# Kernel optimization log

Measured on AMD Instinct MI355X. Metric: run time of the kernel, lower is better.

The kernel has to match this reference:

```python
import jax, jax.numpy as jnp
import numpy as np

N_NODES = 50000
N_EDGES = 800000
D = 128
N_GRAPHS = 64


def setup_inputs() -> dict:
    key = jax.random.key(0)
    ks = jax.random.split(key, 9)
    x = jax.random.normal(ks[0], (N_NODES, D), dtype=jnp.float32)
    edge_index = jax.random.randint(ks[1], (2, N_EDGES), 0, N_NODES, dtype=jnp.int32)
    batch = jnp.sort(jax.random.randint(ks[2], (N_NODES,), 0, N_GRAPHS, dtype=jnp.int32))
    s = 1.0 / np.sqrt(D)
    W1 = jax.random.normal(ks[3], (D, D), jnp.float32) * s
    W2 = jax.random.normal(ks[4], (D, D), jnp.float32) * s
    W3 = jax.random.normal(ks[5], (D, D), jnp.float32) * s
    b1 = jnp.zeros((D,), jnp.float32)
    b2 = jnp.zeros((D,), jnp.float32)
    b3 = jnp.zeros((D,), jnp.float32)
    return {"x": x, "W1": W1, "b1": b1, "W2": W2, "b2": b2, "W3": W3, "b3": b3,
            "edge_index": edge_index, "batch": batch}


def _gcn_conv(x, W, b, src, dst, deg_inv_sqrt):
    # PyG GCNConv: x' = D^{-1/2} (A+I) D^{-1/2} (x W) + b
    h = x @ W                                    # [N, D]
    norm = (deg_inv_sqrt[src] * deg_inv_sqrt[dst])[:, None]   # [E, 1]
    agg = jax.ops.segment_sum(h[src] * norm, dst, num_segments=N_NODES)
    # self-loop contribution: norm_ii = deg_i^{-1}
    agg = agg + (deg_inv_sqrt * deg_inv_sqrt)[:, None] * h
    return agg + b


def reference(x, W1, b1, W2, b2, W3, b3, edge_index, batch):
    src, dst = edge_index[0], edge_index[1]
    # degree on A + I (self-loops added), edge weight 1
    deg = jax.ops.segment_sum(jnp.ones((N_EDGES,), x.dtype), dst,
                              num_segments=N_NODES) + 1.0
    deg_inv_sqrt = jax.lax.rsqrt(deg)
    h = jax.nn.relu(_gcn_conv(x, W1, b1, src, dst, deg_inv_sqrt))
    h = jax.nn.relu(_gcn_conv(h, W2, b2, src, dst, deg_inv_sqrt))
    h = _gcn_conv(h, W3, b3, src, dst, deg_inv_sqrt)
    # global_max_pool over graph ids
    return jax.ops.segment_max(h, batch, num_segments=N_GRAPHS)
```

## Files before the change

kernel.cpp:

```cpp
#include <hip/hip_runtime.h>
#include <float.h>
#include <math.h>

#define D 128
#define PCHUNK 64
#define NBUCK 256
#define BROWS 196
#define BCAP 4096
#define BCAPP 4896
#define ACHUNK 3125

typedef _Float16 half8 __attribute__((ext_vector_type(8)));
typedef _Float16 half2v __attribute__((ext_vector_type(2)));
typedef float f32x4 __attribute__((ext_vector_type(4)));

__device__ __forceinline__ unsigned encf(float x) {
    unsigned u = __float_as_uint(x);
    return (u & 0x80000000u) ? ~u : (u | 0x80000000u);
}
__device__ __forceinline__ float decf(unsigned e) {
    unsigned u = (e & 0x80000000u) ? (e & 0x7FFFFFFFu) : ~e;
    return __uint_as_float(u);
}

__global__ __launch_bounds__(256) void binA_kernel(const int* __restrict__ src,
                                                   const int* __restrict__ dst,
                                                   int* __restrict__ gcnt,
                                                   uint2* __restrict__ gpair, int ne) {
    __shared__ int lh[NBUCK], ssc[NBUCK], lstart[NBUCK], gbase[NBUCK], loff[NBUCK];
    __shared__ uint2 stage[ACHUNK + 8];
    int t = threadIdx.x;
    int e0 = blockIdx.x * ACHUNK;
    int e1 = min(e0 + ACHUNK, ne);
    lh[t] = 0;
    __syncthreads();
    for (int e = e0 + t; e < e1; e += 256) atomicAdd(&lh[dst[e] / BROWS], 1);
    __syncthreads();
    ssc[t] = lh[t];
    __syncthreads();
    for (int off = 1; off < NBUCK; off <<= 1) {
        int u = (t >= off) ? ssc[t - off] : 0;
        __syncthreads();
        ssc[t] += u;
        __syncthreads();
    }
    int st = ssc[t] - lh[t];
    lstart[t] = st;
    loff[t] = st;
    if (lh[t] > 0) gbase[t] = atomicAdd(&gcnt[t], lh[t]);
    __syncthreads();
    for (int e = e0 + t; e < e1; e += 256) {
        int s = src[e], d = dst[e];
        int pos = atomicAdd(&loff[d / BROWS], 1);
        stage[pos] = make_uint2((unsigned)s, (unsigned)d);
    }
    __syncthreads();
    int m = e1 - e0;
    for (int i = t; i < m; i += 256) {
        uint2 pr = stage[i];
        int b = (int)pr.y / BROWS;
        int gpos = b * BCAP + gbase[b] + (i - lstart[b]);
        if (gpos < (b + 1) * BCAP) gpair[gpos] = pr;
    }
}

__global__ __launch_bounds__(256) void binB_kernel(const uint2* __restrict__ gpair,
                                                   const int* __restrict__ gcnt,
                                                   int2* __restrict__ rowptr2,
                                                   float* __restrict__ disv,
                                                   int* __restrict__ csr, int n) {
    __shared__ int lh[256], ssc[256], loff[256];
    __shared__ int cstage[BCAPP];
    int b = blockIdx.x, t = threadIdx.x;
    int m = min(gcnt[b], BCAP);
    int row0 = b * BROWS;
    int nrows = min(BROWS, n - row0);
    if (nrows <= 0) return;
    const uint2* mp = gpair + (size_t)b * BCAP;
    lh[t] = 0;
    __syncthreads();
    for (int i = t; i < m; i += 256) atomicAdd(&lh[(int)mp[i].y - row0], 1);
    __syncthreads();
    int deg = lh[t];
    int pdeg = (deg + 3) & ~3;
    ssc[t] = pdeg;
    __syncthreads();
    for (int off = 1; off < 256; off <<= 1) {
        int u = (t >= off) ? ssc[t - off] : 0;
        __syncthreads();
        ssc[t] += u;
        __syncthreads();
    }
    int st = ssc[t] - pdeg;
    loff[t] = st;
    __syncthreads();
    int bbase = b * BCAPP;
    if (t < nrows) {
        rowptr2[row0 + t] = make_int2(bbase + st, deg);
        disv[row0 + t] = rsqrtf((float)deg + 1.0f);
    }
    for (int i = t; i < m; i += 256) {
        uint2 pr = mp[i];
        int pos = atomicAdd(&loff[(int)pr.y - row0], 1);
        cstage[pos] = (int)pr.x;
    }
    if (t < nrows) {
        for (int k = deg; k < pdeg; k++) cstage[st + k] = row0 + t;
    }
    __syncthreads();
    int ptot = ssc[255];
    for (int i = t; i < ptot; i += 256) csr[bbase + i] = cstage[i];
}

__global__ void pack3_kernel(const float* __restrict__ W1, const float* __restrict__ W2,
                             const float* __restrict__ W3, _Float16* __restrict__ Wp1,
                             _Float16* __restrict__ Wp2, _Float16* __restrict__ Wp3,
                             unsigned* __restrict__ outEnc, int nout) {
    int gi = blockIdx.x * blockDim.x + threadIdx.x;
    if (gi < nout) outEnc[gi] = 0x007FFFFFu;
    int w = gi >> 14, i = gi & 16383;
    const float* W = (w == 0) ? W1 : (w == 1) ? W2 : W3;
    _Float16* Wp = (w == 0) ? Wp1 : (w == 1) ? Wp2 : Wp3;
    int j = i & 7, l = (i >> 3) & 63, t = (i >> 9) & 7, s = (i >> 12) & 3;
    int k = s * 32 + ((l >> 4) << 3) + j;
    int c = t * 16 + (l & 15);
    Wp[i] = (_Float16)W[k * 128 + c];
}

template <bool F32SRC>
__global__ __launch_bounds__(256) void gemm_mfma(const void* __restrict__ Xsrc,
                                                 const _Float16* __restrict__ Wp,
                                                 const float* __restrict__ disv,
                                                 _Float16* __restrict__ Gh,
                                                 int ntiles, int n) {
    __shared__ _Float16 Wl[16384];
    int tid = threadIdx.x;
    {
        const uint4* s4 = (const uint4*)Wp;
        uint4* d4 = (uint4*)Wl;
#pragma unroll
        for (int i = 0; i < 8; i++) d4[tid + 256 * i] = s4[tid + 256 * i];
    }
    __syncthreads();
    int wave = tid >> 6, lane = tid & 63;
    int m = lane & 15, quad = lane >> 4;
    const half8* wfrag = (const half8*)Wl;
    const _Float16* Xh = (const _Float16*)Xsrc;
    const float* Xf = (const float*)Xsrc;

#pragma unroll
    for (int pass = 0; pass < 2; pass++) {
        int tile = blockIdx.x * 8 + pass * 4 + wave;
        if (tile >= ntiles) continue;
        int arow = tile * 16 + m;
        if (arow >= n) arow = n - 1;

        f32x4 acc[8];
#pragma unroll
        for (int t = 0; t < 8; t++) acc[t] = (f32x4){0.f, 0.f, 0.f, 0.f};

#pragma unroll
        for (int s = 0; s < 4; s++) {
            half8 a;
            if (F32SRC) {
                float4 lo = *(const float4*)(Xf + (size_t)arow * D + s * 32 + quad * 8);
                float4 hi = *(const float4*)(Xf + (size_t)arow * D + s * 32 + quad * 8 + 4);
                a[0] = (_Float16)lo.x; a[1] = (_Float16)lo.y; a[2] = (_Float16)lo.z; a[3] = (_Float16)lo.w;
                a[4] = (_Float16)hi.x; a[5] = (_Float16)hi.y; a[6] = (_Float16)hi.z; a[7] = (_Float16)hi.w;
            } else {
                a = *(const half8*)(Xh + (size_t)arow * D + s * 32 + quad * 8);
            }
#pragma unroll
            for (int t = 0; t < 8; t++) {
                half8 bf = wfrag[(s * 8 + t) * 64 + lane];
                acc[t] = __builtin_amdgcn_mfma_f32_16x16x32_f16(a, bf, acc[t], 0, 0, 0);
            }
        }
        int orow0 = tile * 16 + quad * 4;
        if (orow0 + 3 < n) {
            float d0 = disv[orow0], d1 = disv[orow0 + 1], d2 = disv[orow0 + 2], d3 = disv[orow0 + 3];
#pragma unroll
            for (int t = 0; t < 8; t++) {
                int col = t * 16 + m;
                Gh[(size_t)(orow0 + 0) * D + col] = (_Float16)(acc[t][0] * d0);
                Gh[(size_t)(orow0 + 1) * D + col] = (_Float16)(acc[t][1] * d1);
                Gh[(size_t)(orow0 + 2) * D + col] = (_Float16)(acc[t][2] * d2);
                Gh[(size_t)(orow0 + 3) * D + col] = (_Float16)(acc[t][3] * d3);
            }
        } else {
#pragma unroll
            for (int t = 0; t < 8; t++) {
                int col = t * 16 + m;
#pragma unroll
                for (int r = 0; r < 4; r++) {
                    int orow = orow0 + r;
                    if (orow < n) Gh[(size_t)orow * D + col] = (_Float16)(acc[t][r] * disv[orow]);
                }
            }
        }
    }
}

__global__ __launch_bounds__(256) void agg_f16(const _Float16* __restrict__ G,
                                               const int2* __restrict__ rowptr2,
                                               const int* __restrict__ csr,
                                               const float* __restrict__ disv,
                                               const float* __restrict__ bias,
                                               _Float16* __restrict__ Out, int n, int relu) {
    int wave = threadIdx.x >> 6, lane = threadIdx.x & 63;
    int node = blockIdx.x * 4 + wave;
    if (node >= n) return;
    int sub = lane >> 4, li = lane & 15;
    const half8* G8 = (const half8*)G;
    int2 rp = rowptr2[node];
    int e0 = rp.x, deg = rp.y;
    int pend = e0 + ((deg + 3) & ~3);
    int npad = pend - e0 - deg;
    float acc[8];
    if (sub == 0) {
        half8 sv = G8[(size_t)node * 16 + li];
        float w = (float)(1 - npad);
#pragma unroll
        for (int j = 0; j < 8; j++) acc[j] = w * (float)sv[j];
    } else {
#pragma unroll
        for (int j = 0; j < 8; j++) acc[j] = 0.f;
    }
    int e = e0;
    for (; e + 16 <= pend; e += 16) {
        int4 ix = *(const int4*)(csr + e + sub * 4);
        half8 v0 = G8[(size_t)ix.x * 16 + li];
        half8 v1 = G8[(size_t)ix.y * 16 + li];
        half8 v2 = G8[(size_t)ix.z * 16 + li];
        half8 v3 = G8[(size_t)ix.w * 16 + li];
#pragma unroll
        for (int j = 0; j < 8; j++)
            acc[j] += ((float)v0[j] + (float)v1[j]) + ((float)v2[j] + (float)v3[j]);
    }
    if (e + 8 <= pend) {
        int2 ix = *(const int2*)(csr + e + sub * 2);
        half8 v0 = G8[(size_t)ix.x * 16 + li];
        half8 v1 = G8[(size_t)ix.y * 16 + li];
#pragma unroll
        for (int j = 0; j < 8; j++) acc[j] += (float)v0[j] + (float)v1[j];
        e += 8;
    }
    if (e < pend) {
        int i0 = csr[e + sub];
        half8 v0 = G8[(size_t)i0 * 16 + li];
#pragma unroll
        for (int j = 0; j < 8; j++) acc[j] += (float)v0[j];
    }
#pragma unroll
    for (int j = 0; j < 8; j++) {
        acc[j] += __shfl_xor(acc[j], 16);
        acc[j] += __shfl_xor(acc[j], 32);
    }
    if (sub == 0) {
        float dd = disv[node];
        float4 b0 = *(const float4*)&bias[li * 8];
        float4 b1 = *(const float4*)&bias[li * 8 + 4];
        float o0 = fmaf(dd, acc[0], b0.x), o1 = fmaf(dd, acc[1], b0.y);
        float o2 = fmaf(dd, acc[2], b0.z), o3 = fmaf(dd, acc[3], b0.w);
        float o4 = fmaf(dd, acc[4], b1.x), o5 = fmaf(dd, acc[5], b1.y);
        float o6 = fmaf(dd, acc[6], b1.z), o7 = fmaf(dd, acc[7], b1.w);
        if (relu) {
            o0 = fmaxf(o0, 0.f); o1 = fmaxf(o1, 0.f); o2 = fmaxf(o2, 0.f); o3 = fmaxf(o3, 0.f);
            o4 = fmaxf(o4, 0.f); o5 = fmaxf(o5, 0.f); o6 = fmaxf(o6, 0.f); o7 = fmaxf(o7, 0.f);
        }
        half8 h;
        h[0] = (_Float16)o0; h[1] = (_Float16)o1; h[2] = (_Float16)o2; h[3] = (_Float16)o3;
        h[4] = (_Float16)o4; h[5] = (_Float16)o5; h[6] = (_Float16)o6; h[7] = (_Float16)o7;
        ((half8*)Out)[(size_t)node * 16 + li] = h;
    }
}

__global__ __launch_bounds__(128) void pool_kernel(const _Float16* __restrict__ H,
                                                   const int* __restrict__ batch,
                                                   unsigned* __restrict__ outEnc, int n) {
    int half = threadIdx.x >> 6;
    int li = threadIdx.x & 63;
    int start = blockIdx.x * PCHUNK + half * (PCHUNK / 2);
    if (start >= n) return;
    int end = min(start + PCHUNK / 2, n);
    int c = li * 2;
    int curg = batch[start];
    float cx = -INFINITY, cy = -INFINITY;
    for (int i = start; i < end; i++) {
        half2v v = *(const half2v*)(H + (size_t)i * D + c);
        float vx = (float)v[0], vy = (float)v[1];
        int g = batch[i];
        if (g != curg) {
            atomicMax(&outEnc[curg * D + c], encf(cx));
            atomicMax(&outEnc[curg * D + c + 1], encf(cy));
            cx = vx; cy = vy; curg = g;
        } else {
            cx = fmaxf(cx, vx); cy = fmaxf(cy, vy);
        }
    }
    atomicMax(&outEnc[curg * D + c], encf(cx));
    atomicMax(&outEnc[curg * D + c + 1], encf(cy));
}

__global__ void decode_kernel(const unsigned* __restrict__ outEnc, float* __restrict__ out, int n) {
    int i = blockIdx.x * blockDim.x + threadIdx.x;
    if (i < n) out[i] = decf(outEnc[i]);
}

extern "C" void kernel_launch(void* const* d_in, const int* in_sizes, int n_in,
                              void* d_out, int out_size, void* d_ws, size_t ws_size,
                              hipStream_t stream) {
    const float* x  = (const float*)d_in[0];
    const float* W1 = (const float*)d_in[1];
    const float* b1 = (const float*)d_in[2];
    const float* W2 = (const float*)d_in[3];
    const float* b2 = (const float*)d_in[4];
    const float* W3 = (const float*)d_in[5];
    const float* b3 = (const float*)d_in[6];
    const int* ei    = (const int*)d_in[7];
    const int* batch = (const int*)d_in[8];

    int n  = in_sizes[0] / D;
    int ne = in_sizes[7] / 2;
    const int* src = ei;
    const int* dst = ei + ne;

    char* p = (char*)d_ws;
    auto alloc = [&](size_t bytes) -> void* {
        void* q = (void*)p;
        p += (bytes + 255) & ~(size_t)255;
        return q;
    };
    _Float16* Gh  = (_Float16*)alloc((size_t)n * D * 2);
    _Float16* Hh  = (_Float16*)alloc((size_t)n * D * 2);
    _Float16* Wp1 = (_Float16*)alloc((size_t)D * D * 2);
    _Float16* Wp2 = (_Float16*)alloc((size_t)D * D * 2);
    _Float16* Wp3 = (_Float16*)alloc((size_t)D * D * 2);
    int* gcnt     = (int*)alloc((size_t)NBUCK * 4);
    uint2* gpair  = (uint2*)alloc((size_t)NBUCK * BCAP * 8);
    int2* rowptr2 = (int2*)alloc((size_t)n * 8);
    int* csr      = (int*)alloc((size_t)NBUCK * BCAPP * 4);
    float* disv   = (float*)alloc((size_t)n * 4);
    unsigned* outEnc = (unsigned*)alloc((size_t)out_size * 4);

    hipMemsetAsync(gcnt, 0, (size_t)NBUCK * 4, stream);

    int nblocksA = (ne + ACHUNK - 1) / ACHUNK;
    binA_kernel<<<nblocksA, 256, 0, stream>>>(src, dst, gcnt, gpair, ne);
    binB_kernel<<<NBUCK, 256, 0, stream>>>(gpair, gcnt, rowptr2, disv, csr, n);
    pack3_kernel<<<192, 256, 0, stream>>>(W1, W2, W3, Wp1, Wp2, Wp3, outEnc, out_size);

    int ntiles = (n + 15) / 16;
    int gemm_blocks = (ntiles + 7) / 8;
    int agg_blocks  = (n + 3) / 4;

    gemm_mfma<true><<<gemm_blocks, 256, 0, stream>>>(x, Wp1, disv, Gh, ntiles, n);
    agg_f16<<<agg_blocks, 256, 0, stream>>>(Gh, rowptr2, csr, disv, b1, Hh, n, 1);
    gemm_mfma<false><<<gemm_blocks, 256, 0, stream>>>(Hh, Wp2, disv, Gh, ntiles, n);
    agg_f16<<<agg_blocks, 256, 0, stream>>>(Gh, rowptr2, csr, disv, b2, Hh, n, 1);
    gemm_mfma<false><<<gemm_blocks, 256, 0, stream>>>(Hh, Wp3, disv, Gh, ntiles, n);
    agg_f16<<<agg_blocks, 256, 0, stream>>>(Gh, rowptr2, csr, disv, b3, Hh, n, 0);

    pool_kernel<<<(n + PCHUNK - 1) / PCHUNK, 128, 0, stream>>>(Hh, batch, outEnc, n);
    decode_kernel<<<(out_size + 255) / 256, 256, 0, stream>>>(outEnc, (float*)d_out, out_size);
}
```

Before: 248.9 us.

## Merge weight packing into binning launch and add nontemporal hints in aggregation

The weight-packing and output-init work moves into extra blocks of the edge-binning kernel, which removes one kernel launch. The aggregation kernel now uses nontemporal loads for CSR indices and row pointers and nontemporal stores for its output and the CSR writes. It also folds the per-node normalisation into the accumulation as FMAs, in place of a final scale. That adds per-element multiplies and changes rounding slightly, and the nontemporal stores on Out may hurt later GEMM reads that could have hit in cache.

```diff
diff --git a/kernel.cpp b/kernel.cpp
--- a/kernel.cpp
+++ b/kernel.cpp
@@ -13,6 +13,8 @@
 typedef _Float16 half8 __attribute__((ext_vector_type(8)));
 typedef _Float16 half2v __attribute__((ext_vector_type(2)));
 typedef float f32x4 __attribute__((ext_vector_type(4)));
+typedef int i32x4 __attribute__((ext_vector_type(4)));
+typedef int i32x2 __attribute__((ext_vector_type(2)));
 
 __device__ __forceinline__ unsigned encf(float x) {
     unsigned u = __float_as_uint(x);
@@ -23,13 +25,32 @@
     return __uint_as_float(u);
 }
 
-__global__ __launch_bounds__(256) void binA_kernel(const int* __restrict__ src,
-                                                   const int* __restrict__ dst,
-                                                   int* __restrict__ gcnt,
-                                                   uint2* __restrict__ gpair, int ne) {
+__global__ __launch_bounds__(256) void binA_pack(const int* __restrict__ src,
+                                                 const int* __restrict__ dst,
+                                                 int* __restrict__ gcnt,
+                                                 uint2* __restrict__ gpair, int ne, int nblocksA,
+                                                 const float* __restrict__ W1,
+                                                 const float* __restrict__ W2,
+                                                 const float* __restrict__ W3,
+                                                 _Float16* __restrict__ Wp1,
+                                                 _Float16* __restrict__ Wp2,
+                                                 _Float16* __restrict__ Wp3,
+                                                 unsigned* __restrict__ outEnc, int nout) {
+    int t = threadIdx.x;
+    if (blockIdx.x >= nblocksA) {
+        int gi = (blockIdx.x - nblocksA) * 256 + t;
+        if (gi < nout) outEnc[gi] = 0x007FFFFFu;
+        int w = gi >> 14, i = gi & 16383;
+        const float* W = (w == 0) ? W1 : (w == 1) ? W2 : W3;
+        _Float16* Wp = (w == 0) ? Wp1 : (w == 1) ? Wp2 : Wp3;
+        int j = i & 7, l = (i >> 3) & 63, tt = (i >> 9) & 7, s = (i >> 12) & 3;
+        int k = s * 32 + ((l >> 4) << 3) + j;
+        int c = tt * 16 + (l & 15);
+        Wp[i] = (_Float16)W[k * 128 + c];
+        return;
+    }
     __shared__ int lh[NBUCK], ssc[NBUCK], lstart[NBUCK], gbase[NBUCK], loff[NBUCK];
     __shared__ uint2 stage[ACHUNK + 8];
-    int t = threadIdx.x;
     int e0 = blockIdx.x * ACHUNK;
     int e1 = min(e0 + ACHUNK, ne);
     lh[t] = 0;
@@ -109,22 +130,8 @@
     }
     __syncthreads();
     int ptot = ssc[255];
-    for (int i = t; i < ptot; i += 256) csr[bbase + i] = cstage[i];
-}
-
-__global__ void pack3_kernel(const float* __restrict__ W1, const float* __restrict__ W2,
-                             const float* __restrict__ W3, _Float16* __restrict__ Wp1,
-                             _Float16* __restrict__ Wp2, _Float16* __restrict__ Wp3,
-                             unsigned* __restrict__ outEnc, int nout) {
-    int gi = blockIdx.x * blockDim.x + threadIdx.x;
-    if (gi < nout) outEnc[gi] = 0x007FFFFFu;
-    int w = gi >> 14, i = gi & 16383;
-    const float* W = (w == 0) ? W1 : (w == 1) ? W2 : W3;
-    _Float16* Wp = (w == 0) ? Wp1 : (w == 1) ? Wp2 : Wp3;
-    int j = i & 7, l = (i >> 3) & 63, t = (i >> 9) & 7, s = (i >> 12) & 3;
-    int k = s * 32 + ((l >> 4) << 3) + j;
-    int c = t * 16 + (l & 15);
-    Wp[i] = (_Float16)W[k * 128 + c];
+    for (int i = t; i < ptot; i += 256)
+        __builtin_nontemporal_store(cstage[i], &csr[bbase + i]);
 }
 
 template <bool F32SRC>
@@ -212,14 +219,15 @@
     if (node >= n) return;
     int sub = lane >> 4, li = lane & 15;
     const half8* G8 = (const half8*)G;
-    int2 rp = rowptr2[node];
-    int e0 = rp.x, deg = rp.y;
+    long long rpll = __builtin_nontemporal_load((const long long*)(rowptr2 + node));
+    int e0 = (int)(unsigned)rpll, deg = (int)(rpll >> 32);
+    float dd = disv[node];
     int pend = e0 + ((deg + 3) & ~3);
     int npad = pend - e0 - deg;
     float acc[8];
     if (sub == 0) {
         half8 sv = G8[(size_t)node * 16 + li];
-        float w = (float)(1 - npad);
+        float w = (float)(1 - npad) * dd;
 #pragma unroll
         for (int j = 0; j < 8; j++) acc[j] = w * (float)sv[j];
     } else {
@@ -228,28 +236,35 @@
     }
     int e = e0;
     for (; e + 16 <= pend; e += 16) {
-        int4 ix = *(const int4*)(csr + e + sub * 4);
-        half8 v0 = G8[(size_t)ix.x * 16 + li];
-        half8 v1 = G8[(size_t)ix.y * 16 + li];
-        half8 v2 = G8[(size_t)ix.z * 16 + li];
-        half8 v3 = G8[(size_t)ix.w * 16 + li];
-#pragma unroll
-        for (int j = 0; j < 8; j++)
-            acc[j] += ((float)v0[j] + (float)v1[j]) + ((float)v2[j] + (float)v3[j]);
+        i32x4 ix = __builtin_nontemporal_load((const i32x4*)(csr + e + sub * 4));
+        half8 v0 = G8[(size_t)ix[0] * 16 + li];
+        half8 v1 = G8[(size_t)ix[1] * 16 + li];
+        half8 v2 = G8[(size_t)ix[2] * 16 + li];
+        half8 v3 = G8[(size_t)ix[3] * 16 + li];
+#pragma unroll
+        for (int j = 0; j < 8; j++) {
+            acc[j] = fmaf((float)v0[j], dd, acc[j]);
+            acc[j] = fmaf((float)v1[j], dd, acc[j]);
+            acc[j] = fmaf((float)v2[j], dd, acc[j]);
+            acc[j] = fmaf((float)v3[j], dd, acc[j]);
+        }
     }
     if (e + 8 <= pend) {
-        int2 ix = *(const int2*)(csr + e + sub * 2);
-        half8 v0 = G8[(size_t)ix.x * 16 + li];
-        half8 v1 = G8[(size_t)ix.y * 16 + li];
-#pragma unroll
-        for (int j = 0; j < 8; j++) acc[j] += (float)v0[j] + (float)v1[j];
+        i32x2 ix = __builtin_nontemporal_load((const i32x2*)(csr + e + sub * 2));
+        half8 v0 = G8[(size_t)ix[0] * 16 + li];
+        half8 v1 = G8[(size_t)ix[1] * 16 + li];
+#pragma unroll
+        for (int j = 0; j < 8; j++) {
+            acc[j] = fmaf((float)v0[j], dd, acc[j]);
+            acc[j] = fmaf((float)v1[j], dd, acc[j]);
+        }
         e += 8;
     }
     if (e < pend) {
-        int i0 = csr[e + sub];
+        int i0 = __builtin_nontemporal_load(csr + e + sub);
         half8 v0 = G8[(size_t)i0 * 16 + li];
 #pragma unroll
-        for (int j = 0; j < 8; j++) acc[j] += (float)v0[j];
+        for (int j = 0; j < 8; j++) acc[j] = fmaf((float)v0[j], dd, acc[j]);
     }
 #pragma unroll
     for (int j = 0; j < 8; j++) {
@@ -257,13 +272,12 @@
         acc[j] += __shfl_xor(acc[j], 32);
     }
     if (sub == 0) {
-        float dd = disv[node];
         float4 b0 = *(const float4*)&bias[li * 8];
         float4 b1 = *(const float4*)&bias[li * 8 + 4];
-        float o0 = fmaf(dd, acc[0], b0.x), o1 = fmaf(dd, acc[1], b0.y);
-        float o2 = fmaf(dd, acc[2], b0.z), o3 = fmaf(dd, acc[3], b0.w);
-        float o4 = fmaf(dd, acc[4], b1.x), o5 = fmaf(dd, acc[5], b1.y);
-        float o6 = fmaf(dd, acc[6], b1.z), o7 = fmaf(dd, acc[7], b1.w);
+        float o0 = acc[0] + b0.x, o1 = acc[1] + b0.y;
+        float o2 = acc[2] + b0.z, o3 = acc[3] + b0.w;
+        float o4 = acc[4] + b1.x, o5 = acc[5] + b1.y;
+        float o6 = acc[6] + b1.z, o7 = acc[7] + b1.w;
         if (relu) {
             o0 = fmaxf(o0, 0.f); o1 = fmaxf(o1, 0.f); o2 = fmaxf(o2, 0.f); o3 = fmaxf(o3, 0.f);
             o4 = fmaxf(o4, 0.f); o5 = fmaxf(o5, 0.f); o6 = fmaxf(o6, 0.f); o7 = fmaxf(o7, 0.f);
@@ -271,7 +285,7 @@
         half8 h;
         h[0] = (_Float16)o0; h[1] = (_Float16)o1; h[2] = (_Float16)o2; h[3] = (_Float16)o3;
         h[4] = (_Float16)o4; h[5] = (_Float16)o5; h[6] = (_Float16)o6; h[7] = (_Float16)o7;
-        ((half8*)Out)[(size_t)node * 16 + li] = h;
+        __builtin_nontemporal_store(h, (half8*)Out + (size_t)node * 16 + li);
     }
 }
 
@@ -346,9 +360,9 @@
     hipMemsetAsync(gcnt, 0, (size_t)NBUCK * 4, stream);
 
     int nblocksA = (ne + ACHUNK - 1) / ACHUNK;
-    binA_kernel<<<nblocksA, 256, 0, stream>>>(src, dst, gcnt, gpair, ne);
+    binA_pack<<<nblocksA + 192, 256, 0, stream>>>(src, dst, gcnt, gpair, ne, nblocksA,
+                                                  W1, W2, W3, Wp1, Wp2, Wp3, outEnc, out_size);
     binB_kernel<<<NBUCK, 256, 0, stream>>>(gpair, gcnt, rowptr2, disv, csr, n);
-    pack3_kernel<<<192, 256, 0, stream>>>(W1, W2, W3, Wp1, Wp2, Wp3, outEnc, out_size);
 
     int ntiles = (n + 15) / 16;
     int gemm_blocks = (ntiles + 7) / 8;
```

Result: slower. 263.9 us (+6.0%).
